# Optimization experiments

Measured on AMD Instinct MI355X. Metric: run time of the kernel, lower is better.

The kernel has to match this reference:

```python
import jax, jax.numpy as jnp
import numpy as np

N = 100_000
E = 1_600_000
C_IN, C_HID, C_OUT = 128, 128, 64


def setup_inputs() -> dict:
    key = jax.random.key(0)
    ks = jax.random.split(key, 10)
    inp = {
        "x": jax.random.normal(ks[0], (N, C_IN), dtype=jnp.float32),
        "edge_index": jax.random.randint(ks[1], (2, E), 0, N, dtype=jnp.int64),
        "edge_weight": jax.random.uniform(ks[2], (E,), dtype=jnp.float32),
        # learned params: 2 hidden GCN layers + output GCN layer (glorot-ish scale)
        "W1": jax.random.normal(ks[3], (C_IN, C_HID), dtype=jnp.float32) / np.sqrt(C_IN),
        "b1": jnp.zeros((C_HID,), dtype=jnp.float32),
        "W2": jax.random.normal(ks[4], (C_HID, C_HID), dtype=jnp.float32) / np.sqrt(C_HID),
        "b2": jnp.zeros((C_HID,), dtype=jnp.float32),
        "W3": jax.random.normal(ks[5], (C_HID, C_OUT), dtype=jnp.float32) / np.sqrt(C_HID),
        "b3": jnp.zeros((C_OUT,), dtype=jnp.float32),
    }
    return inp


def _gcn_conv(x, src, dst, w, W, b):
    # PyG GCNConv: h = X @ W; out[j] = sum_{(i->j)} norm_ij * h[i] + b
    # norm_ij = deg_i^{-1/2} * w_ij * deg_j^{-1/2}, deg = weighted in-degree (incl. self loops)
    h = x @ W                                      # [N, out]
    deg = jax.ops.segment_sum(w, dst, num_segments=N)  # [N]
    dinv = jnp.where(deg > 0, jax.lax.rsqrt(deg), 0.0)
    norm = dinv[src] * w * dinv[dst]               # [E']
    msg = h[src] * norm[:, None]                   # [E', out] gather-scale
    out = jax.ops.segment_sum(msg, dst, num_segments=N)  # scatter-add
    return out + b


def reference(x, edge_index, edge_weight, W1, b1, W2, b2, W3, b3):
    # add self loops once (weight 1.0), as GCNConv does per layer
    loop = jnp.arange(N, dtype=edge_index.dtype)
    src = jnp.concatenate([edge_index[0], loop])
    dst = jnp.concatenate([edge_index[1], loop])
    w = jnp.concatenate([edge_weight, jnp.ones((N,), dtype=edge_weight.dtype)])

    h = _gcn_conv(x, src, dst, w, W1, b1)
    h = jax.nn.relu(h)          # Dropout is identity in eval mode
    h = _gcn_conv(h, src, dst, w, W2, b2)
    h = jax.nn.relu(h)
    out = _gcn_conv(h, src, dst, w, W3, b3)
    return out
```

## Files before the change

kernel.cpp:

```cpp
#include <hip/hip_runtime.h>
#include <cstdint>
#include <cstddef>

#define TPB 256

__device__ __forceinline__ unsigned short f2bf(float f) {
  unsigned u = __float_as_uint(f);
  u += 0x7fffu + ((u >> 16) & 1u);
  return (unsigned short)(u >> 16);
}
__device__ __forceinline__ float bf_lo(unsigned u) { return __uint_as_float(u << 16); }
__device__ __forceinline__ float bf_hi(unsigned u) { return __uint_as_float(u & 0xffff0000u); }

#define FIXP32 8192.0f
#define DEGMASK 0xFFFFFu

typedef __attribute__((ext_vector_type(8))) short  short8v;
typedef __attribute__((ext_vector_type(4))) float  float4v;


template<int COUT, bool RELU, bool BF16IN>
__device__ __forceinline__ void gemm_body(int bid, const void* __restrict__ Xv,
                                          const unsigned short* __restrict__ Wt,
                                          unsigned short* __restrict__ H, int n) {
  const int lane = threadIdx.x & 63;
  const int wv   = threadIdx.x >> 6;
  const int r0   = (bid * 4 + wv) * 16;
  if (r0 >= n) return;
  const int c16   = lane & 15;
  const int kb    = (lane >> 4) * 8;
  const int row_c = min(r0 + c16, n - 1);

  short8v a[4];
  if (BF16IN) {
    const unsigned short* xrow = (const unsigned short*)Xv + (size_t)row_c * 128;
    #pragma unroll
    for (int kk = 0; kk < 4; kk++) {
      short8v t = *(const short8v*)(xrow + kk * 32 + kb);
      if (RELU) {
        #pragma unroll
        for (int j = 0; j < 8; j++) t[j] = (short)(t[j] & 0x8000) ? (short)0 : t[j];
      }
      a[kk] = t;
    }
  } else {
    const float* xrow = (const float*)Xv + (size_t)row_c * 128;
    #pragma unroll
    for (int kk = 0; kk < 4; kk++) {
      float4 lo = *(const float4*)(xrow + kk * 32 + kb);
      float4 hi = *(const float4*)(xrow + kk * 32 + kb + 4);
      float v0 = lo.x, v1 = lo.y, v2 = lo.z, v3 = lo.w;
      float v4 = hi.x, v5 = hi.y, v6 = hi.z, v7 = hi.w;
      if (RELU) {
        v0 = fmaxf(v0, 0.f); v1 = fmaxf(v1, 0.f); v2 = fmaxf(v2, 0.f); v3 = fmaxf(v3, 0.f);
        v4 = fmaxf(v4, 0.f); v5 = fmaxf(v5, 0.f); v6 = fmaxf(v6, 0.f); v7 = fmaxf(v7, 0.f);
      }
      short8v t;
      t[0] = (short)f2bf(v0); t[1] = (short)f2bf(v1);
      t[2] = (short)f2bf(v2); t[3] = (short)f2bf(v3);
      t[4] = (short)f2bf(v4); t[5] = (short)f2bf(v5);
      t[6] = (short)f2bf(v6); t[7] = (short)f2bf(v7);
      a[kk] = t;
    }
  }

  constexpr int CT = COUT / 16;
  const int orow = r0 + (lane >> 4) * 4;
  #pragma unroll
  for (int ct = 0; ct < CT; ct++) {
    float4v acc = {0.f, 0.f, 0.f, 0.f};
    const unsigned short* wrow = Wt + (size_t)(ct * 16 + c16) * 128 + kb;
    #pragma unroll
    for (int kk = 0; kk < 4; kk++) {
      short8v b = *(const short8v*)(wrow + kk * 32);
      acc = __builtin_amdgcn_mfma_f32_16x16x32_bf16(a[kk], b, acc, 0, 0, 0);
    }
    const int ocol = ct * 16 + c16;
    #pragma unroll
    for (int r = 0; r < 4; r++) {
      if (orow + r < n)
        H[(size_t)(orow + r) * COUT + ocol] = f2bf(acc[r]);
    }
  }
}


__global__ __launch_bounds__(256) void fused_edges_gemm1(
    const int* __restrict__ ei, const float* __restrict__ w,
    unsigned* __restrict__ pk, int* __restrict__ pir, int E, int eb,
    const float* __restrict__ X, const unsigned short* __restrict__ Wt,
    unsigned short* __restrict__ H, int n, int gb) {
  const int q = blockIdx.x / 5;
  const int r = blockIdx.x % 5;
  if (r < 4) {
    int eid = q * 4 + r;
    if (eid >= eb) return;
    int e = eid * TPB + threadIdx.x;
    if (e >= E) return;
    int d = ei[E + e];
    unsigned v = (1u << 20) | (unsigned)(w[e] * FIXP32 + 0.5f);
    unsigned old = atomicAdd(&pk[d], v);
    pir[e] = (int)(old >> 20);
  } else {
    if (q >= gb) return;
    gemm_body<128, false, false>(q, X, Wt, H, n);
  }
}

__global__ void scan_a(const unsigned* __restrict__ pk, float* __restrict__ dinv,
                       int* __restrict__ rp, int* __restrict__ bsum, int n) {
  __shared__ int s[TPB];
  int i = blockIdx.x * TPB + threadIdx.x;
  unsigned pv = (i < n) ? pk[i] : 0u;
  if (i < n)
    dinv[i] = rsqrtf(1.0f + (float)(pv & DEGMASK) * (1.0f / FIXP32));
  int v = (int)(pv >> 20);
  s[threadIdx.x] = v;
  __syncthreads();
  #pragma unroll
  for (int off = 1; off < TPB; off <<= 1) {
    int t = (threadIdx.x >= off) ? s[threadIdx.x - off] : 0;
    __syncthreads();
    s[threadIdx.x] += t;
    __syncthreads();
  }
  if (i < n) rp[i] = s[threadIdx.x] - v;
  if (threadIdx.x == TPB - 1) bsum[blockIdx.x] = s[TPB - 1];
}

__global__ void scan_b(int* __restrict__ bsum, int nb) {
  __shared__ int s[512];
  int v = (threadIdx.x < nb) ? bsum[threadIdx.x] : 0;
  s[threadIdx.x] = v;
  __syncthreads();
  #pragma unroll
  for (int off = 1; off < 512; off <<= 1) {
    int t = (threadIdx.x >= off) ? s[threadIdx.x - off] : 0;
    __syncthreads();
    s[threadIdx.x] += t;
    __syncthreads();
  }
  if (threadIdx.x < nb) bsum[threadIdx.x] = s[threadIdx.x] - v;
}

__global__ void scan_c(int* __restrict__ rp, const int* __restrict__ bsum, int n, int etot) {
  int i = blockIdx.x * TPB + threadIdx.x;
  if (i < n) rp[i] += bsum[blockIdx.x];
  if (blockIdx.x == 0 && threadIdx.x == 0) rp[n] = etot;
}

__global__ void fill_k(const int* __restrict__ ei, const float* __restrict__ w,
                       const float* __restrict__ dinv, const int* __restrict__ rp,
                       const int* __restrict__ pir, int2* __restrict__ epk, int E) {
  int e = blockIdx.x * TPB + threadIdx.x;
  if (e >= E) return;
  int s = ei[e];
  int d = ei[E + e];
  int pos = rp[d] + pir[e];
  float nrm = dinv[s] * w[e] * dinv[d];
  epk[pos] = make_int2(s, __float_as_int(nrm));
}

__global__ void wt_k(const float* __restrict__ W1, const float* __restrict__ W2,
                     const float* __restrict__ W3,
                     unsigned short* __restrict__ wt1, unsigned short* __restrict__ wt2,
                     unsigned short* __restrict__ wt3) {
  int t = blockIdx.x * TPB + threadIdx.x;
  if (t < 16384) {
    int c = t >> 7, k = t & 127;
    wt1[t] = f2bf(W1[k * 128 + c]);
  } else if (t < 32768) {
    int u = t - 16384;
    int c = u >> 7, k = u & 127;
    wt2[u] = f2bf(W2[k * 128 + c]);
  } else if (t < 40960) {
    int u = t - 32768;
    int c = u >> 7, k = u & 127;
    wt3[u] = f2bf(W3[k * 64 + c]);
  }
}

template<int COUT, bool RELU, bool BF16IN>
__global__ __launch_bounds__(256) void gemm_mfma(const void* __restrict__ Xv,
                                                 const unsigned short* __restrict__ Wt,
                                                 unsigned short* __restrict__ H, int n) {
  gemm_body<COUT, RELU, BF16IN>(blockIdx.x, Xv, Wt, H, n);
}


__global__ __launch_bounds__(256) void agg128(const unsigned short* __restrict__ H,
                                              const int* __restrict__ rp,
                                              const int2* __restrict__ epk,
                                              const float* __restrict__ dinv,
                                              const float* __restrict__ bias,
                                              unsigned* __restrict__ OUT, int n) {
  int wid  = __builtin_amdgcn_readfirstlane(blockIdx.x * 4 + (threadIdx.x >> 6));
  int lane = threadIdx.x & 63;
  if (wid >= n) return;
  float di = dinv[wid];
  float w0 = di * di;
  unsigned hv = ((const unsigned*)(H + (size_t)wid * 128))[lane];
  float2 bv = ((const float2*)bias)[lane];
  float ax = bv.x + w0 * bf_lo(hv);
  float ay = bv.y + w0 * bf_hi(hv);
  int e  = rp[wid];
  int e1 = rp[wid + 1];
  for (; e + 15 < e1; e += 16) {
    int2 p[16];
    #pragma unroll
    for (int u = 0; u < 16; u++) p[u] = epk[e + u];
    unsigned h[16];
    #pragma unroll
    for (int u = 0; u < 16; u++) h[u] = ((const unsigned*)(H + (size_t)p[u].x * 128))[lane];
    #pragma unroll
    for (int u = 0; u < 16; u++) {
      float nw = __int_as_float(p[u].y);
      ax += nw * bf_lo(h[u]);
      ay += nw * bf_hi(h[u]);
    }
  }
  for (; e + 3 < e1; e += 4) {
    int2 p[4];
    #pragma unroll
    for (int u = 0; u < 4; u++) p[u] = epk[e + u];
    unsigned h[4];
    #pragma unroll
    for (int u = 0; u < 4; u++) h[u] = ((const unsigned*)(H + (size_t)p[u].x * 128))[lane];
    #pragma unroll
    for (int u = 0; u < 4; u++) {
      float nw = __int_as_float(p[u].y);
      ax += nw * bf_lo(h[u]);
      ay += nw * bf_hi(h[u]);
    }
  }
  for (; e < e1; e++) {
    int2 p = epk[e];
    unsigned h = ((const unsigned*)(H + (size_t)p.x * 128))[lane];
    float nw = __int_as_float(p.y);
    ax += nw * bf_lo(h); ay += nw * bf_hi(h);
  }
  OUT[(size_t)wid * 64 + lane] = (unsigned)f2bf(ax) | ((unsigned)f2bf(ay) << 16);
}

__global__ __launch_bounds__(256) void agg64(const unsigned short* __restrict__ H,
                                             const int* __restrict__ rp,
                                             const int2* __restrict__ epk,
                                             const float* __restrict__ dinv,
                                             const float* __restrict__ bias,
                                             float* __restrict__ OUT, int n) {
  int wid  = __builtin_amdgcn_readfirstlane(blockIdx.x * 4 + (threadIdx.x >> 6));
  int lane = threadIdx.x & 63;
  if (wid >= n) return;
  float di = dinv[wid];
  float w0 = di * di;
  float hv = __uint_as_float(((unsigned)H[(size_t)wid * 64 + lane]) << 16);
  float acc = bias[lane] + w0 * hv;
  int e  = rp[wid];
  int e1 = rp[wid + 1];
  for (; e + 15 < e1; e += 16) {
    int2 p[16];
    #pragma unroll
    for (int u = 0; u < 16; u++) p[u] = epk[e + u];
    float h[16];
    #pragma unroll
    for (int u = 0; u < 16; u++)
      h[u] = __uint_as_float(((unsigned)H[(size_t)p[u].x * 64 + lane]) << 16);
    #pragma unroll
    for (int u = 0; u < 16; u++) acc += __int_as_float(p[u].y) * h[u];
  }
  for (; e + 3 < e1; e += 4) {
    int2 p[4];
    #pragma unroll
    for (int u = 0; u < 4; u++) p[u] = epk[e + u];
    float h[4];
    #pragma unroll
    for (int u = 0; u < 4; u++)
      h[u] = __uint_as_float(((unsigned)H[(size_t)p[u].x * 64 + lane]) << 16);
    #pragma unroll
    for (int u = 0; u < 4; u++) acc += __int_as_float(p[u].y) * h[u];
  }
  for (; e < e1; e++) {
    int2 p = epk[e];
    float h = __uint_as_float(((unsigned)H[(size_t)p.x * 64 + lane]) << 16);
    acc += __int_as_float(p.y) * h;
  }
  OUT[(size_t)wid * 64 + lane] = acc;
}


extern "C" void kernel_launch(void* const* d_in, const int* in_sizes, int n_in,
                              void* d_out, int out_size, void* d_ws, size_t ws_size,
                              hipStream_t stream) {
  const float* x  = (const float*)d_in[0];
  const int*   ei = (const int*)d_in[1];
  const float* ew = (const float*)d_in[2];
  const float* W1 = (const float*)d_in[3];
  const float* b1 = (const float*)d_in[4];
  const float* W2 = (const float*)d_in[5];
  const float* b2 = (const float*)d_in[6];
  const float* W3 = (const float*)d_in[7];
  const float* b3 = (const float*)d_in[8];

  const int N = in_sizes[0] / 128;
  const int E = in_sizes[2];

  char* p = (char*)d_ws;
  auto carve = [&](size_t bytes) -> void* {
    void* r = (void*)p;
    p += (bytes + 255) & ~(size_t)255;
    return r;
  };
  unsigned* pk  = (unsigned*)carve((size_t)N * 4);
  float* dinv   = (float*)carve((size_t)N * 4);
  int*   rp     = (int*)  carve((size_t)(N + 1) * 4);
  int*   bsum   = (int*)  carve(512 * 4);
  int*   pir    = (int*)  carve((size_t)E * 4);
  int2*  epk    = (int2*) carve((size_t)E * 8);
  unsigned short* hbuf = (unsigned short*)carve((size_t)N * 128 * 2);
  unsigned* abuf = (unsigned*)carve((size_t)N * 128 * 2);
  unsigned short* wt1 = (unsigned short*)carve(16384 * 2);
  unsigned short* wt2 = (unsigned short*)carve(16384 * 2);
  unsigned short* wt3 = (unsigned short*)carve(8192 * 2);

  const int NB = (N + TPB - 1) / TPB;
  const int EB = (E + TPB - 1) / TPB;
  const int aggBlocks  = (N + 3) / 4;
  const int gemmBlocks = (N + 63) / 64;

  hipMemsetAsync(pk, 0, (size_t)N * 4, stream);
  wt_k<<<160, TPB, 0, stream>>>(W1, W2, W3, wt1, wt2, wt3);
  int periods = (EB + 3) / 4;
  if (gemmBlocks > periods) periods = gemmBlocks;
  fused_edges_gemm1<<<5 * periods + 5, TPB, 0, stream>>>(
      ei, ew, pk, pir, E, EB, x, wt1, hbuf, N, gemmBlocks);
  scan_a<<<NB, TPB, 0, stream>>>(pk, dinv, rp, bsum, N);
  scan_b<<<1, 512, 0, stream>>>(bsum, NB);
  scan_c<<<NB, TPB, 0, stream>>>(rp, bsum, N, E);
  fill_k<<<EB, TPB, 0, stream>>>(ei, ew, dinv, rp, pir, epk, E);

  agg128<<<aggBlocks, 256, 0, stream>>>(hbuf, rp, epk, dinv, b1, abuf, N);

  gemm_mfma<128, true, true><<<gemmBlocks, 256, 0, stream>>>(abuf, wt2, hbuf, N);
  agg128<<<aggBlocks, 256, 0, stream>>>(hbuf, rp, epk, dinv, b2, abuf, N);

  gemm_mfma<64, true, true><<<gemmBlocks, 256, 0, stream>>>(abuf, wt3, hbuf, N);
  agg64<<<aggBlocks, 256, 0, stream>>>(hbuf, rp, epk, dinv, b3, (float*)d_out, N);
}
```

Measured before the change: 344.4 us.

## Fuse neighbor aggregation with following MFMA GEMM via shared-memory tile

Replaces the separate agg128 and gemm_mfma launches with one agg_gemm kernel. Each block aggregates 16 nodes (4 per wave), stages the bf16 rows in LDS with ReLU applied, then runs the 16x16x32 bf16 MFMA against the transposed weights and writes the next layer's features. This removes the intermediate aggregated buffer's global write and re-read plus two kernel launches. In exchange, each wave walks 4 node rows serially, which may reduce latency hiding for the gather, and each block re-reads the full weight matrix from cache.

```diff
diff --git a/kernel.cpp b/kernel.cpp
--- a/kernel.cpp
+++ b/kernel.cpp
@@ -180,67 +180,107 @@
   }
 }
 
-template<int COUT, bool RELU, bool BF16IN>
-__global__ __launch_bounds__(256) void gemm_mfma(const void* __restrict__ Xv,
-                                                 const unsigned short* __restrict__ Wt,
-                                                 unsigned short* __restrict__ H, int n) {
-  gemm_body<COUT, RELU, BF16IN>(blockIdx.x, Xv, Wt, H, n);
-}
-
-
-__global__ __launch_bounds__(256) void agg128(const unsigned short* __restrict__ H,
-                                              const int* __restrict__ rp,
-                                              const int2* __restrict__ epk,
-                                              const float* __restrict__ dinv,
-                                              const float* __restrict__ bias,
-                                              unsigned* __restrict__ OUT, int n) {
-  int wid  = __builtin_amdgcn_readfirstlane(blockIdx.x * 4 + (threadIdx.x >> 6));
-  int lane = threadIdx.x & 63;
-  if (wid >= n) return;
-  float di = dinv[wid];
-  float w0 = di * di;
-  unsigned hv = ((const unsigned*)(H + (size_t)wid * 128))[lane];
-  float2 bv = ((const float2*)bias)[lane];
-  float ax = bv.x + w0 * bf_lo(hv);
-  float ay = bv.y + w0 * bf_hi(hv);
-  int e  = rp[wid];
-  int e1 = rp[wid + 1];
-  for (; e + 15 < e1; e += 16) {
-    int2 p[16];
-    #pragma unroll
-    for (int u = 0; u < 16; u++) p[u] = epk[e + u];
-    unsigned h[16];
-    #pragma unroll
-    for (int u = 0; u < 16; u++) h[u] = ((const unsigned*)(H + (size_t)p[u].x * 128))[lane];
-    #pragma unroll
-    for (int u = 0; u < 16; u++) {
-      float nw = __int_as_float(p[u].y);
-      ax += nw * bf_lo(h[u]);
-      ay += nw * bf_hi(h[u]);
-    }
-  }
-  for (; e + 3 < e1; e += 4) {
-    int2 p[4];
-    #pragma unroll
-    for (int u = 0; u < 4; u++) p[u] = epk[e + u];
-    unsigned h[4];
-    #pragma unroll
-    for (int u = 0; u < 4; u++) h[u] = ((const unsigned*)(H + (size_t)p[u].x * 128))[lane];
-    #pragma unroll
-    for (int u = 0; u < 4; u++) {
-      float nw = __int_as_float(p[u].y);
-      ax += nw * bf_lo(h[u]);
-      ay += nw * bf_hi(h[u]);
-    }
-  }
-  for (; e < e1; e++) {
-    int2 p = epk[e];
-    unsigned h = ((const unsigned*)(H + (size_t)p.x * 128))[lane];
-    float nw = __int_as_float(p.y);
-    ax += nw * bf_lo(h); ay += nw * bf_hi(h);
-  }
-  OUT[(size_t)wid * 64 + lane] = (unsigned)f2bf(ax) | ((unsigned)f2bf(ay) << 16);
-}
+
+#define ASTRIDE 136
+
+template<int COUT>
+__global__ __launch_bounds__(256) void agg_gemm(const unsigned short* __restrict__ H,
+                                                const int* __restrict__ rp,
+                                                const int2* __restrict__ epk,
+                                                const float* __restrict__ dinv,
+                                                const float* __restrict__ bias,
+                                                const unsigned short* __restrict__ Wt,
+                                                unsigned short* __restrict__ Hout, int n) {
+  __shared__ unsigned short As[16 * ASTRIDE];
+  const int lane = threadIdx.x & 63;
+  const int wv   = threadIdx.x >> 6;
+  const int base = blockIdx.x * 16;
+  if (base >= n) return;
+
+  for (int i = 0; i < 4; i++) {
+    int node = base + wv * 4 + i;
+    if (node >= n) break;
+    float di = dinv[node];
+    float w0 = di * di;
+    unsigned hv = ((const unsigned*)(H + (size_t)node * 128))[lane];
+    float2 bv = ((const float2*)bias)[lane];
+    float ax = bv.x + w0 * bf_lo(hv);
+    float ay = bv.y + w0 * bf_hi(hv);
+    int e  = rp[node];
+    int e1 = rp[node + 1];
+    for (; e + 15 < e1; e += 16) {
+      int2 p[16];
+      #pragma unroll
+      for (int u = 0; u < 16; u++) p[u] = epk[e + u];
+      unsigned h[16];
+      #pragma unroll
+      for (int u = 0; u < 16; u++) h[u] = ((const unsigned*)(H + (size_t)p[u].x * 128))[lane];
+      #pragma unroll
+      for (int u = 0; u < 16; u++) {
+        float nw = __int_as_float(p[u].y);
+        ax += nw * bf_lo(h[u]);
+        ay += nw * bf_hi(h[u]);
+      }
+    }
+    for (; e + 3 < e1; e += 4) {
+      int2 p[4];
+      #pragma unroll
+      for (int u = 0; u < 4; u++) p[u] = epk[e + u];
+      unsigned h[4];
+      #pragma unroll
+      for (int u = 0; u < 4; u++) h[u] = ((const unsigned*)(H + (size_t)p[u].x * 128))[lane];
+      #pragma unroll
+      for (int u = 0; u < 4; u++) {
+        float nw = __int_as_float(p[u].y);
+        ax += nw * bf_lo(h[u]);
+        ay += nw * bf_hi(h[u]);
+      }
+    }
+    for (; e < e1; e++) {
+      int2 p = epk[e];
+      unsigned h = ((const unsigned*)(H + (size_t)p.x * 128))[lane];
+      float nw = __int_as_float(p.y);
+      ax += nw * bf_lo(h); ay += nw * bf_hi(h);
+    }
+    unsigned pk2 = (unsigned)f2bf(ax) | ((unsigned)f2bf(ay) << 16);
+    *(unsigned*)(As + (wv * 4 + i) * ASTRIDE + lane * 2) = pk2;
+  }
+  __syncthreads();
+
+  constexpr int CT  = COUT / 16;
+  constexpr int TPW = CT / 4;
+  const int c16  = lane & 15;
+  const int kb   = (lane >> 4) * 8;
+  const int vrow = min(16, n - base);
+  const int rrow = min(c16, vrow - 1);
+  short8v a[4];
+  #pragma unroll
+  for (int kk = 0; kk < 4; kk++) {
+    short8v t = *(const short8v*)(As + rrow * ASTRIDE + kk * 32 + kb);
+    #pragma unroll
+    for (int j = 0; j < 8; j++) t[j] = (short)(t[j] & 0x8000) ? (short)0 : t[j];
+    a[kk] = t;
+  }
+  const int orow0 = base + (lane >> 4) * 4;
+  #pragma unroll
+  for (int tt = 0; tt < TPW; tt++) {
+    const int ct = wv * TPW + tt;
+    float4v acc = {0.f, 0.f, 0.f, 0.f};
+    const unsigned short* wrow = Wt + (size_t)(ct * 16 + c16) * 128 + kb;
+    #pragma unroll
+    for (int kk = 0; kk < 4; kk++) {
+      short8v b = *(const short8v*)(wrow + kk * 32);
+      acc = __builtin_amdgcn_mfma_f32_16x16x32_bf16(a[kk], b, acc, 0, 0, 0);
+    }
+    const int ocol = ct * 16 + c16;
+    #pragma unroll
+    for (int r = 0; r < 4; r++) {
+      if (orow0 + r < n)
+        Hout[(size_t)(orow0 + r) * COUT + ocol] = f2bf(acc[r]);
+    }
+  }
+}
+
 
 __global__ __launch_bounds__(256) void agg64(const unsigned short* __restrict__ H,
                                              const int* __restrict__ rp,
@@ -316,16 +356,17 @@
   int*   bsum   = (int*)  carve(512 * 4);
   int*   pir    = (int*)  carve((size_t)E * 4);
   int2*  epk    = (int2*) carve((size_t)E * 8);
-  unsigned short* hbuf = (unsigned short*)carve((size_t)N * 128 * 2);
-  unsigned* abuf = (unsigned*)carve((size_t)N * 128 * 2);
+  unsigned short* hbuf  = (unsigned short*)carve((size_t)N * 128 * 2);
+  unsigned short* hbuf2 = (unsigned short*)carve((size_t)N * 128 * 2);
   unsigned short* wt1 = (unsigned short*)carve(16384 * 2);
   unsigned short* wt2 = (unsigned short*)carve(16384 * 2);
   unsigned short* wt3 = (unsigned short*)carve(8192 * 2);
 
   const int NB = (N + TPB - 1) / TPB;
   const int EB = (E + TPB - 1) / TPB;
+  const int gemmBlocks = (N + 63) / 64;
+  const int agBlocks   = (N + 15) / 16;
   const int aggBlocks  = (N + 3) / 4;
-  const int gemmBlocks = (N + 63) / 64;
 
   hipMemsetAsync(pk, 0, (size_t)N * 4, stream);
   wt_k<<<160, TPB, 0, stream>>>(W1, W2, W3, wt1, wt2, wt3);
@@ -338,11 +379,9 @@
   scan_c<<<NB, TPB, 0, stream>>>(rp, bsum, N, E);
   fill_k<<<EB, TPB, 0, stream>>>(ei, ew, dinv, rp, pir, epk, E);
 
-  agg128<<<aggBlocks, 256, 0, stream>>>(hbuf, rp, epk, dinv, b1, abuf, N);
-
-  gemm_mfma<128, true, true><<<gemmBlocks, 256, 0, stream>>>(abuf, wt2, hbuf, N);
-  agg128<<<aggBlocks, 256, 0, stream>>>(hbuf, rp, epk, dinv, b2, abuf, N);
-
-  gemm_mfma<64, true, true><<<gemmBlocks, 256, 0, stream>>>(abuf, wt3, hbuf, N);
+  agg_gemm<128><<<agBlocks, 256, 0, stream>>>(hbuf, rp, epk, dinv, b1, wt2, hbuf2, N);
+
+  agg_gemm<64><<<agBlocks, 256, 0, stream>>>(hbuf2, rp, epk, dinv, b2, wt3, hbuf, N);
+
   agg64<<<aggBlocks, 256, 0, stream>>>(hbuf, rp, epk, dinv, b3, (float*)d_out, N);
 }
```

After: 352.9 us. 1.02x slower.
